# Kernel optimization log

Measured on AMD Instinct MI355X. Metric: run time of the kernel, lower is better.

Reference implementation:

```python
import jax, jax.numpy as jnp
import numpy as np

N = 50000      # nodes
E = 1600000    # edges (avg degree 32)
D = 128        # in_features
H = 2          # heads
C = 64         # out channels per head (hidden_dims[i])
HC = H * C     # concat dim per layer


def _gtc_layer(x, src, dst, Wq, bq, Wk, bk, Wv, bv, Ws, bs, gamma, beta):
    """PyG TransformerConv (concat heads, root skip) + LayerNorm."""
    n = x.shape[0]
    q = (x @ Wq + bq).reshape(n, H, C)   # [N,H,C]
    k = (x @ Wk + bk).reshape(n, H, C)
    v = (x @ Wv + bv).reshape(n, H, C)
    # per-edge attention logits: query at target, key at source
    alpha = (q[dst] * k[src]).sum(-1) * (1.0 / np.sqrt(C))  # [E,H]
    # segment softmax over incoming edges of each target node
    amax = jax.ops.segment_max(alpha, dst, num_segments=n)   # [N,H]
    ex = jnp.exp(alpha - amax[dst])                          # [E,H]
    denom = jax.ops.segment_sum(ex, dst, num_segments=n)     # [N,H]
    w = ex / denom[dst]                                      # [E,H]
    # weighted scatter-sum of source values
    out = jax.ops.segment_sum(v[src] * w[:, :, None], dst, num_segments=n)
    out = out.reshape(n, HC) + (x @ Ws + bs)  # root skip (lin_skip)
    # LayerNorm (eps=1e-5)
    mu = out.mean(-1, keepdims=True)
    var = ((out - mu) ** 2).mean(-1, keepdims=True)
    return gamma * (out - mu) / jnp.sqrt(var + 1e-5) + beta


def setup_inputs() -> dict:
    key = jax.random.key(0)
    ks = jax.random.split(key, 24)
    x = jax.random.normal(ks[0], (N, D), dtype=jnp.float32)
    edge_index = jax.random.randint(ks[1], (2, E), 0, N, dtype=jnp.int32)
    inp = {"x": x, "edge_index": edge_index}
    dims = [(D, HC), (HC, HC)]  # layer0: 128->128, layer1: 128->128
    ki = 2
    for li, (din, dout) in enumerate(dims):
        s = 1.0 / np.sqrt(din)
        for nm in ("Wq", "Wk", "Wv", "Ws"):
            inp[f"{nm}{li}"] = jax.random.uniform(ks[ki], (din, dout), jnp.float32, -s, s); ki += 1
        for nm in ("bq", "bk", "bv", "bs"):
            inp[f"{nm}{li}"] = jax.random.uniform(ks[ki], (dout,), jnp.float32, -s, s); ki += 1
        inp[f"g{li}"] = jnp.ones((dout,), jnp.float32)
        inp[f"be{li}"] = jnp.zeros((dout,), jnp.float32)
    return inp


def reference(x, edge_index,
              Wq0, Wk0, Wv0, Ws0, bq0, bk0, bv0, bs0, g0, be0,
              Wq1, Wk1, Wv1, Ws1, bq1, bk1, bv1, bs1, g1, be1):
    src, dst = edge_index[0], edge_index[1]
    h = _gtc_layer(x, src, dst, Wq0, bq0, Wk0, bk0, Wv0, bv0, Ws0, bs0, g0, be0)
    h = _gtc_layer(h, src, dst, Wq1, bq1, Wk1, bk1, Wv1, bv1, Ws1, bs1, g1, be1)
    return h
```

## Files before the change

### kernel.cpp

```cpp
#include <hip/hip_runtime.h>
#include <math.h>

#define NN 50000
#define NE 1600000
#define NBIN 391
#define BINCAP 4608
#define EPB 8192

typedef __attribute__((ext_vector_type(8))) short bf16x8;
typedef __attribute__((ext_vector_type(4))) float f32x4;
typedef __attribute__((ext_vector_type(2))) float f32x2;

__device__ __forceinline__ ushort f2bf(float f) {
  union { float f; unsigned u; } a; a.f = f;
  return (ushort)((a.u + 0x7fffu + ((a.u >> 16) & 1u)) >> 16);
}
__device__ __forceinline__ f32x2 unp2(unsigned u) {
  f32x2 r;
  r.x = __uint_as_float(u << 16);
  r.y = __uint_as_float(u & 0xffff0000u);
  return r;
}

__global__ __launch_bounds__(256) void prep_weights(
    const float* __restrict__ Wq0, const float* __restrict__ Wk0,
    const float* __restrict__ Wv0, const float* __restrict__ Ws0,
    const float* __restrict__ bq0, const float* __restrict__ bk0,
    const float* __restrict__ bv0, const float* __restrict__ bs0,
    const float* __restrict__ Wq1, const float* __restrict__ Wk1,
    const float* __restrict__ Wv1, const float* __restrict__ Ws1,
    const float* __restrict__ bq1, const float* __restrict__ bk1,
    const float* __restrict__ bv1, const float* __restrict__ bs1,
    ushort* __restrict__ Wt0, ushort* __restrict__ Wt1,
    float* __restrict__ bias0, float* __restrict__ bias1)
{
  int idx = blockIdx.x * 256 + threadIdx.x;
  if (idx >= 2 * 512 * 128) return;
  const int layer = idx >> 16;
  const int li = idx & 0xFFFF;
  const int n = li >> 7, k = li & 127, g = n >> 7, nl = n & 127;
  const float* W;
  if (layer == 0) W = g == 0 ? Wq0 : g == 1 ? Wk0 : g == 2 ? Wv0 : Ws0;
  else            W = g == 0 ? Wq1 : g == 1 ? Wk1 : g == 2 ? Wv1 : Ws1;
  (layer == 0 ? Wt0 : Wt1)[li] = f2bf(W[k * 128 + nl]);
  if (li < 512) {
    const int gb = li >> 7, nb = li & 127;
    const float* B;
    if (layer == 0) B = gb == 0 ? bq0 : gb == 1 ? bk0 : gb == 2 ? bv0 : bs0;
    else            B = gb == 0 ? bq1 : gb == 1 ? bk1 : gb == 2 ? bv1 : bs1;
    (layer == 0 ? bias0 : bias1)[li] = B[nb];
  }
}

template <int AF32>
__global__ __launch_bounds__(512) void gemm_v2(
    const void* __restrict__ Av, const ushort* __restrict__ Wt,
    const float* __restrict__ bias,
    ushort* __restrict__ q_bf, ushort* __restrict__ s_bf,
    unsigned char* __restrict__ kv8, int M)
{
  __shared__ char As[128 * 256];
  const int t = threadIdx.x;
  const int m0 = blockIdx.x * 128;

  #pragma unroll
  for (int it = 0; it < 4; ++it) {
    const int L = it * 4096 + t * 8;
    const int row = L >> 7, col = L & 127;
    const int grow = m0 + row;
    uint4 pk = make_uint4(0, 0, 0, 0);
    if (grow < M) {
      if (AF32) {
        const float* ap = (const float*)Av + (size_t)grow * 128 + col;
        const float4 a = *(const float4*)ap;
        const float4 b = *(const float4*)(ap + 4);
        pk.x = (unsigned)f2bf(a.x) | ((unsigned)f2bf(a.y) << 16);
        pk.y = (unsigned)f2bf(a.z) | ((unsigned)f2bf(a.w) << 16);
        pk.z = (unsigned)f2bf(b.x) | ((unsigned)f2bf(b.y) << 16);
        pk.w = (unsigned)f2bf(b.z) | ((unsigned)f2bf(b.w) << 16);
      } else {
        pk = *(const uint4*)((const ushort*)Av + (size_t)grow * 128 + col);
      }
    }
    const int byte = (row * 256 + col * 2) ^ ((row & 7) << 4);
    *(uint4*)(As + byte) = pk;
  }
  __syncthreads();

  const int w = t >> 6, l = t & 63, lr = l & 15, lk = l >> 4;
  const int nb = w * 64;
  const int g = w >> 1;

  bf16x8 bfr[4][4];
  #pragma unroll
  for (int ni = 0; ni < 4; ++ni)
    #pragma unroll
    for (int kk = 0; kk < 4; ++kk)
      bfr[ni][kk] = *(const bf16x8*)(Wt + (size_t)(nb + ni * 16 + lr) * 128 + kk * 32 + lk * 8);
  float4 b4[4];
  #pragma unroll
  for (int ni = 0; ni < 4; ++ni)
    b4[ni] = *(const float4*)(bias + nb + ni * 16 + lk * 4);

  #pragma unroll
  for (int mi = 0; mi < 8; ++mi) {
    const int r = mi * 16 + lr;
    bf16x8 af[4];
    #pragma unroll
    for (int kk = 0; kk < 4; ++kk) {
      const int byte = (r * 256 + (kk * 32 + lk * 8) * 2) ^ ((r & 7) << 4);
      af[kk] = *(const bf16x8*)(As + byte);
    }
    f32x4 acc[4];
    #pragma unroll
    for (int ni = 0; ni < 4; ++ni) acc[ni] = (f32x4){0.f, 0.f, 0.f, 0.f};
    #pragma unroll
    for (int kk = 0; kk < 4; ++kk)
      #pragma unroll
      for (int ni = 0; ni < 4; ++ni)
        acc[ni] = __builtin_amdgcn_mfma_f32_16x16x32_bf16(bfr[ni][kk], af[kk], acc[ni], 0, 0, 0);

    const int row = m0 + mi * 16 + lr;
    if (row < M) {
      #pragma unroll
      for (int ni = 0; ni < 4; ++ni) {
        const float v0 = acc[ni][0] + b4[ni].x;
        const float v1 = acc[ni][1] + b4[ni].y;
        const float v2 = acc[ni][2] + b4[ni].z;
        const float v3 = acc[ni][3] + b4[ni].w;
        const int c = (nb & 127) + ni * 16 + lk * 4;
        if (g == 0 || g == 3) {
          ushort4 o4;
          o4.x = f2bf(v0); o4.y = f2bf(v1); o4.z = f2bf(v2); o4.w = f2bf(v3);
          ushort* dstp = (g == 0) ? q_bf : s_bf;
          *(ushort4*)(dstp + (size_t)row * 128 + c) = o4;
        } else {
          unsigned u = __builtin_amdgcn_cvt_pk_fp8_f32(v0, v1, 0, false);
          u = __builtin_amdgcn_cvt_pk_fp8_f32(v2, v3, u, true);
          *(unsigned*)(kv8 + (size_t)row * 256 + (g == 2 ? 128 : 0) + c) = u;
        }
      }
    }
  }
}

__global__ __launch_bounds__(256) void bin_scatter(
    const int* __restrict__ src, const int* __restrict__ dst,
    int* __restrict__ binCnt, unsigned* __restrict__ binbuf, int E)
{
  __shared__ int hist[NBIN];
  __shared__ int base[NBIN];
  const int t = threadIdx.x;
  const int e0 = blockIdx.x * EPB;
  const int e1 = min(e0 + EPB, E);
  for (int i = t; i < NBIN; i += 256) hist[i] = 0;
  __syncthreads();
  for (int e = e0 + t; e < e1; e += 256) atomicAdd(&hist[dst[e] >> 7], 1);
  __syncthreads();
  for (int i = t; i < NBIN; i += 256) {
    const int c = hist[i];
    base[i] = (c > 0) ? atomicAdd(&binCnt[i], c) : 0;
    hist[i] = 0;
  }
  __syncthreads();
  for (int e = e0 + t; e < e1; e += 256) {
    const int d = dst[e], b = d >> 7;
    const int p = base[b] + atomicAdd(&hist[b], 1);
    if (p < BINCAP)
      binbuf[(size_t)b * BINCAP + p] = (unsigned)src[e] | ((unsigned)(d & 127) << 16);
  }
}

__global__ __launch_bounds__(256) void bin_fill(
    const unsigned* __restrict__ binbuf, const int* __restrict__ binCnt,
    int* __restrict__ row_start, int* __restrict__ colv)
{
  __shared__ int hist[128], scanb[128], cur[128];
  __shared__ int wred[4];
  const int b = blockIdx.x, t = threadIdx.x;
  int part = 0;
  for (int i = t; i < b; i += 256) part += min(binCnt[i], BINCAP);
  #pragma unroll
  for (int o = 32; o; o >>= 1) part += __shfl_xor(part, o, 64);
  if ((t & 63) == 0) wred[t >> 6] = part;
  const int n = min(binCnt[b], BINCAP);
  const unsigned* __restrict__ buf = binbuf + (size_t)b * BINCAP;
  if (t < 128) hist[t] = 0;
  __syncthreads();
  const int binBase = wred[0] + wred[1] + wred[2] + wred[3];
  if (b == NBIN - 1 && t == 0) row_start[NN] = binBase + n;
  for (int i = t; i < n; i += 256) atomicAdd(&hist[(buf[i] >> 16) & 127], 1);
  __syncthreads();
  if (t < 128) scanb[t] = hist[t];
  __syncthreads();
  for (int off = 1; off < 128; off <<= 1) {
    int a = (t >= off && t < 128) ? scanb[t - off] : 0;
    __syncthreads();
    if (t < 128) scanb[t] += a;
    __syncthreads();
  }
  if (t < 128) {
    const int node = b * 128 + t;
    const int base = binBase + scanb[t] - hist[t];
    if (node < NN) row_start[node] = base;
    cur[t] = base;
  }
  __syncthreads();
  for (int i = t; i < n; i += 256) {
    const unsigned v = buf[i];
    const int pos = atomicAdd(&cur[(v >> 16) & 127], 1);
    colv[pos] = (int)(v & 0xFFFFu);
  }
}

template <int WRITE_BF16>
__global__ __launch_bounds__(256) void edge_attn(
    const ushort* __restrict__ q_bf, const ushort* __restrict__ s_bf,
    const unsigned char* __restrict__ kv8,
    const int* __restrict__ row_start, const int* __restrict__ colv,
    const float* __restrict__ gamma, const float* __restrict__ beta,
    float* __restrict__ out_f, ushort* __restrict__ out_bf)
{
  const int wave = threadIdx.x >> 6, lane = threadIdx.x & 63;
  const int e8 = lane >> 3, l8 = lane & 7;
  const int n = blockIdx.x * 4 + wave;
  if (n >= NN) return;
  const int beg = row_start[n];
  const int deg = row_start[n + 1] - beg;

  int sn_own = 0;
  const bool small = (deg <= 64);
  if (small && deg > 0) sn_own = colv[beg + min(lane, deg - 1)];

  f32x2 qv[8];
  {
    const uint4 qa = *(const uint4*)(q_bf + (size_t)n * 128 + l8 * 16);
    const uint4 qb = *(const uint4*)(q_bf + (size_t)n * 128 + l8 * 16 + 8);
    qv[0] = unp2(qa.x); qv[1] = unp2(qa.y); qv[2] = unp2(qa.z); qv[3] = unp2(qa.w);
    qv[4] = unp2(qb.x); qv[5] = unp2(qb.y); qv[6] = unp2(qb.z); qv[7] = unp2(qb.w);
  }

  f32x2 acc2[8];
  #pragma unroll
  for (int j = 0; j < 8; ++j) acc2[j] = (f32x2){0.f, 0.f};
  float den = 0.f;

  #pragma unroll 4
  for (int base = 0; base < deg; base += 8) {
    const int i = base + e8;
    const int ii = min(i, deg - 1);
    const int sn = small ? __shfl(sn_own, ii, 64) : colv[beg + ii];
    const unsigned char* kvp = kv8 + (size_t)sn * 256 + l8 * 16;
    const uint4 kw = *(const uint4*)kvp;
    const uint4 vw = *(const uint4*)(kvp + 128);
    f32x2 p2 = __builtin_amdgcn_cvt_pk_f32_fp8((int)kw.x, false) * qv[0];
    p2 += __builtin_amdgcn_cvt_pk_f32_fp8((int)kw.x, true)  * qv[1];
    p2 += __builtin_amdgcn_cvt_pk_f32_fp8((int)kw.y, false) * qv[2];
    p2 += __builtin_amdgcn_cvt_pk_f32_fp8((int)kw.y, true)  * qv[3];
    p2 += __builtin_amdgcn_cvt_pk_f32_fp8((int)kw.z, false) * qv[4];
    p2 += __builtin_amdgcn_cvt_pk_f32_fp8((int)kw.z, true)  * qv[5];
    p2 += __builtin_amdgcn_cvt_pk_f32_fp8((int)kw.w, false) * qv[6];
    p2 += __builtin_amdgcn_cvt_pk_f32_fp8((int)kw.w, true)  * qv[7];
    float p = p2.x + p2.y;
    p += __shfl_xor(p, 1, 64);
    p += __shfl_xor(p, 2, 64);
    const float e = (i < deg) ? __expf(p * 0.125f) : 0.f;
    den += e;
    const f32x2 e2 = (f32x2){e, e};
    acc2[0] += __builtin_amdgcn_cvt_pk_f32_fp8((int)vw.x, false) * e2;
    acc2[1] += __builtin_amdgcn_cvt_pk_f32_fp8((int)vw.x, true)  * e2;
    acc2[2] += __builtin_amdgcn_cvt_pk_f32_fp8((int)vw.y, false) * e2;
    acc2[3] += __builtin_amdgcn_cvt_pk_f32_fp8((int)vw.y, true)  * e2;
    acc2[4] += __builtin_amdgcn_cvt_pk_f32_fp8((int)vw.z, false) * e2;
    acc2[5] += __builtin_amdgcn_cvt_pk_f32_fp8((int)vw.z, true)  * e2;
    acc2[6] += __builtin_amdgcn_cvt_pk_f32_fp8((int)vw.w, false) * e2;
    acc2[7] += __builtin_amdgcn_cvt_pk_f32_fp8((int)vw.w, true)  * e2;
  }

  #pragma unroll
  for (int off = 8; off <= 32; off <<= 1) {
    den += __shfl_xor(den, off, 64);
    #pragma unroll
    for (int j = 0; j < 8; ++j) {
      acc2[j].x += __shfl_xor(acc2[j].x, off, 64);
      acc2[j].y += __shfl_xor(acc2[j].y, off, 64);
    }
  }

  const float rden = (deg > 0) ? 1.f / den : 0.f;
  float o[16], s1 = 0.f, s2 = 0.f;
  {
    const uint4 ra = *(const uint4*)(s_bf + (size_t)n * 128 + l8 * 16);
    const uint4 rb = *(const uint4*)(s_bf + (size_t)n * 128 + l8 * 16 + 8);
    f32x2 sv[8];
    sv[0] = unp2(ra.x); sv[1] = unp2(ra.y); sv[2] = unp2(ra.z); sv[3] = unp2(ra.w);
    sv[4] = unp2(rb.x); sv[5] = unp2(rb.y); sv[6] = unp2(rb.z); sv[7] = unp2(rb.w);
    #pragma unroll
    for (int j = 0; j < 8; ++j) {
      const float a = acc2[j].x * rden + sv[j].x;
      const float b = acc2[j].y * rden + sv[j].y;
      o[2 * j] = a; o[2 * j + 1] = b;
      s1 += a + b; s2 += a * a + b * b;
    }
  }
  #pragma unroll
  for (int off = 1; off <= 4; off <<= 1) {
    s1 += __shfl_xor(s1, off, 64);
    s2 += __shfl_xor(s2, off, 64);
  }
  const float mean = s1 * (1.f / 128.f);
  const float var  = s2 * (1.f / 128.f) - mean * mean;
  const float rs   = rsqrtf(fmaxf(var, 0.f) + 1e-5f);
  if (e8 == 0) {
    const int cbase = l8 * 16;
    #pragma unroll
    for (int jj = 0; jj < 4; ++jj) {
      const float4 g4 = *(const float4*)(gamma + cbase + jj * 4);
      const float4 b4 = *(const float4*)(beta + cbase + jj * 4);
      const float r0 = g4.x * ((o[jj*4+0] - mean) * rs) + b4.x;
      const float r1 = g4.y * ((o[jj*4+1] - mean) * rs) + b4.y;
      const float r2 = g4.z * ((o[jj*4+2] - mean) * rs) + b4.z;
      const float r3 = g4.w * ((o[jj*4+3] - mean) * rs) + b4.w;
      if (WRITE_BF16) {
        ushort4 u4; u4.x = f2bf(r0); u4.y = f2bf(r1); u4.z = f2bf(r2); u4.w = f2bf(r3);
        *(ushort4*)(out_bf + (size_t)n * 128 + cbase + jj * 4) = u4;
      } else {
        *(float4*)(out_f + (size_t)n * 128 + cbase + jj * 4) = make_float4(r0, r1, r2, r3);
      }
    }
  }
}

extern "C" void kernel_launch(void* const* d_in, const int* in_sizes, int n_in,
                              void* d_out, int out_size, void* d_ws, size_t ws_size,
                              hipStream_t stream)
{
  const float* x  = (const float*)d_in[0];
  const int*   ei = (const int*)d_in[1];
  const float* P[20];
  for (int i = 0; i < 20; ++i) P[i] = (const float*)d_in[2 + i];

  char* w = (char*)d_ws;
  ushort* q_bf = (ushort*)w; w += (size_t)NN * 128 * 2;
  ushort* s_bf = (ushort*)w; w += (size_t)NN * 128 * 2;
  unsigned char* kv8 = (unsigned char*)w; w += (size_t)NN * 256;
  ushort* h_bf = (ushort*)w; w += (size_t)NN * 128 * 2;
  unsigned* binbuf = (unsigned*)w; w += (size_t)NBIN * BINCAP * 4;
  int* colv = (int*)w;      w += (size_t)NE * 4;
  ushort* Wt0 = (ushort*)w; w += (size_t)512 * 128 * 2;
  ushort* Wt1 = (ushort*)w; w += (size_t)512 * 128 * 2;
  float* bias0 = (float*)w; w += 512 * 4;
  float* bias1 = (float*)w; w += 512 * 4;
  int* row_start = (int*)w; w += (size_t)(NN + 1) * 4;
  int* binCnt = (int*)w;    w += (size_t)NBIN * 4;

  const int* srcv = ei;
  const int* dstv = ei + NE;

  hipMemsetAsync(binCnt, 0, (size_t)NBIN * 4, stream);
  bin_scatter<<<(NE + EPB - 1) / EPB, 256, 0, stream>>>(srcv, dstv, binCnt, binbuf, NE);
  bin_fill<<<NBIN, 256, 0, stream>>>(binbuf, binCnt, row_start, colv);

  prep_weights<<<(2 * 512 * 128 + 255) / 256, 256, 0, stream>>>(
      P[0], P[1], P[2], P[3], P[4], P[5], P[6], P[7],
      P[10], P[11], P[12], P[13], P[14], P[15], P[16], P[17],
      Wt0, Wt1, bias0, bias1);

  const int ggrid = (NN + 127) / 128;
  const int agrid = (NN + 3) / 4;

  gemm_v2<1><<<ggrid, 512, 0, stream>>>(x, Wt0, bias0, q_bf, s_bf, kv8, NN);
  edge_attn<1><<<agrid, 256, 0, stream>>>(q_bf, s_bf, kv8, row_start, colv,
                                          P[8], P[9], nullptr, h_bf);
  gemm_v2<0><<<ggrid, 512, 0, stream>>>(h_bf, Wt1, bias1, q_bf, s_bf, kv8, NN);
  edge_attn<0><<<agrid, 256, 0, stream>>>(q_bf, s_bf, kv8, row_start, colv,
                                          P[18], P[19], (float*)d_out, nullptr);
}
```

Before: 238.3 us.

## Merge independent preprocessing kernels into fat launches and process two nodes per wave

Bin scatter and weight prep are merged into one launch, and the layer-0 GEMM and CSR bin fill are merged into another, with blocks split by blockIdx so the independent work runs concurrently. This cuts launch count and lets the two stages fill each other's idle CUs. Each wave in edge attention now handles two destination nodes. The softmax scale is folded into q with log2e so exp2f replaces __expf. The fat kernels force 512-thread blocks and a 32KB LDS footprint on the fill path, which may reduce occupancy for those blocks.

```diff
diff --git a/kernel.cpp b/kernel.cpp
--- a/kernel.cpp
+++ b/kernel.cpp
@@ -6,10 +6,15 @@
 #define NBIN 391
 #define BINCAP 4608
 #define EPB 8192
+#define SCAT_B ((NE + EPB - 1) / EPB)
+#define PREP_B (2 * 512 * 128 / 512)
+#define GEMM_B ((NN + 127) / 128)
 
 typedef __attribute__((ext_vector_type(8))) short bf16x8;
 typedef __attribute__((ext_vector_type(4))) float f32x4;
 typedef __attribute__((ext_vector_type(2))) float f32x2;
+
+struct WPtrs { const float* p[16]; };
 
 __device__ __forceinline__ ushort f2bf(float f) {
   union { float f; unsigned u; } a; a.f = f;
@@ -22,46 +27,15 @@
   return r;
 }
 
-__global__ __launch_bounds__(256) void prep_weights(
-    const float* __restrict__ Wq0, const float* __restrict__ Wk0,
-    const float* __restrict__ Wv0, const float* __restrict__ Ws0,
-    const float* __restrict__ bq0, const float* __restrict__ bk0,
-    const float* __restrict__ bv0, const float* __restrict__ bs0,
-    const float* __restrict__ Wq1, const float* __restrict__ Wk1,
-    const float* __restrict__ Wv1, const float* __restrict__ Ws1,
-    const float* __restrict__ bq1, const float* __restrict__ bk1,
-    const float* __restrict__ bv1, const float* __restrict__ bs1,
-    ushort* __restrict__ Wt0, ushort* __restrict__ Wt1,
-    float* __restrict__ bias0, float* __restrict__ bias1)
-{
-  int idx = blockIdx.x * 256 + threadIdx.x;
-  if (idx >= 2 * 512 * 128) return;
-  const int layer = idx >> 16;
-  const int li = idx & 0xFFFF;
-  const int n = li >> 7, k = li & 127, g = n >> 7, nl = n & 127;
-  const float* W;
-  if (layer == 0) W = g == 0 ? Wq0 : g == 1 ? Wk0 : g == 2 ? Wv0 : Ws0;
-  else            W = g == 0 ? Wq1 : g == 1 ? Wk1 : g == 2 ? Wv1 : Ws1;
-  (layer == 0 ? Wt0 : Wt1)[li] = f2bf(W[k * 128 + nl]);
-  if (li < 512) {
-    const int gb = li >> 7, nb = li & 127;
-    const float* B;
-    if (layer == 0) B = gb == 0 ? bq0 : gb == 1 ? bk0 : gb == 2 ? bv0 : bs0;
-    else            B = gb == 0 ? bq1 : gb == 1 ? bk1 : gb == 2 ? bv1 : bs1;
-    (layer == 0 ? bias0 : bias1)[li] = B[nb];
-  }
-}
-
 template <int AF32>
-__global__ __launch_bounds__(512) void gemm_v2(
+__device__ __forceinline__ void gemm_body(
     const void* __restrict__ Av, const ushort* __restrict__ Wt,
     const float* __restrict__ bias,
     ushort* __restrict__ q_bf, ushort* __restrict__ s_bf,
-    unsigned char* __restrict__ kv8, int M)
-{
-  __shared__ char As[128 * 256];
+    unsigned char* __restrict__ kv8, int M, char* As, int bid)
+{
   const int t = threadIdx.x;
-  const int m0 = blockIdx.x * 128;
+  const int m0 = bid * 128;
 
   #pragma unroll
   for (int it = 0; it < 4; ++it) {
@@ -144,42 +118,70 @@
   }
 }
 
-__global__ __launch_bounds__(256) void bin_scatter(
+__global__ __launch_bounds__(512) void fat_scatter_prep(
     const int* __restrict__ src, const int* __restrict__ dst,
-    int* __restrict__ binCnt, unsigned* __restrict__ binbuf, int E)
-{
-  __shared__ int hist[NBIN];
-  __shared__ int base[NBIN];
+    int* __restrict__ binCnt, unsigned* __restrict__ binbuf,
+    WPtrs wp,
+    ushort* __restrict__ Wt0, ushort* __restrict__ Wt1,
+    float* __restrict__ bias0, float* __restrict__ bias1)
+{
   const int t = threadIdx.x;
-  const int e0 = blockIdx.x * EPB;
-  const int e1 = min(e0 + EPB, E);
-  for (int i = t; i < NBIN; i += 256) hist[i] = 0;
-  __syncthreads();
-  for (int e = e0 + t; e < e1; e += 256) atomicAdd(&hist[dst[e] >> 7], 1);
-  __syncthreads();
-  for (int i = t; i < NBIN; i += 256) {
-    const int c = hist[i];
-    base[i] = (c > 0) ? atomicAdd(&binCnt[i], c) : 0;
-    hist[i] = 0;
-  }
-  __syncthreads();
-  for (int e = e0 + t; e < e1; e += 256) {
-    const int d = dst[e], b = d >> 7;
-    const int p = base[b] + atomicAdd(&hist[b], 1);
-    if (p < BINCAP)
-      binbuf[(size_t)b * BINCAP + p] = (unsigned)src[e] | ((unsigned)(d & 127) << 16);
-  }
-}
-
-__global__ __launch_bounds__(256) void bin_fill(
+  if (blockIdx.x < SCAT_B) {
+    __shared__ int hist[NBIN], base[NBIN];
+    const int e0 = blockIdx.x * EPB;
+    const int e1 = min(e0 + EPB, NE);
+    for (int i = t; i < NBIN; i += 512) hist[i] = 0;
+    __syncthreads();
+    for (int e = e0 + t; e < e1; e += 512) atomicAdd(&hist[dst[e] >> 7], 1);
+    __syncthreads();
+    for (int i = t; i < NBIN; i += 512) {
+      const int c = hist[i];
+      base[i] = (c > 0) ? atomicAdd(&binCnt[i], c) : 0;
+      hist[i] = 0;
+    }
+    __syncthreads();
+    for (int e = e0 + t; e < e1; e += 512) {
+      const int d = dst[e], b = d >> 7;
+      const int p = base[b] + atomicAdd(&hist[b], 1);
+      if (p < BINCAP)
+        binbuf[(size_t)b * BINCAP + p] = (unsigned)src[e] | ((unsigned)(d & 127) << 16);
+    }
+  } else {
+    const int idx = (blockIdx.x - SCAT_B) * 512 + t;
+    const int layer = idx >> 16;
+    const int li = idx & 0xFFFF;
+    const int n = li >> 7, k = li & 127, g = n >> 7, nl = n & 127;
+    const float* W = wp.p[layer * 8 + g];
+    (layer == 0 ? Wt0 : Wt1)[li] = f2bf(W[k * 128 + nl]);
+    if (li < 512) {
+      const int gb = li >> 7, nbv = li & 127;
+      const float* B = wp.p[layer * 8 + 4 + gb];
+      (layer == 0 ? bias0 : bias1)[li] = B[nbv];
+    }
+  }
+}
+
+__global__ __launch_bounds__(512) void fat_gemm_fill(
+    const float* __restrict__ x, const ushort* __restrict__ Wt0,
+    const float* __restrict__ bias0,
+    ushort* __restrict__ q_bf, ushort* __restrict__ s_bf,
+    unsigned char* __restrict__ kv8,
     const unsigned* __restrict__ binbuf, const int* __restrict__ binCnt,
     int* __restrict__ row_start, int* __restrict__ colv)
 {
-  __shared__ int hist[128], scanb[128], cur[128];
-  __shared__ int wred[4];
-  const int b = blockIdx.x, t = threadIdx.x;
+  __shared__ char smem[128 * 256];
+  const int t = threadIdx.x;
+  if (blockIdx.x < GEMM_B) {
+    gemm_body<1>(x, Wt0, bias0, q_bf, s_bf, kv8, NN, smem, blockIdx.x);
+    return;
+  }
+  int* hist  = (int*)smem;
+  int* scanb = hist + 128;
+  int* cur   = scanb + 128;
+  int* wred  = cur + 128;
+  const int b = blockIdx.x - GEMM_B;
   int part = 0;
-  for (int i = t; i < b; i += 256) part += min(binCnt[i], BINCAP);
+  for (int i = t; i < b; i += 512) part += min(binCnt[i], BINCAP);
   #pragma unroll
   for (int o = 32; o; o >>= 1) part += __shfl_xor(part, o, 64);
   if ((t & 63) == 0) wred[t >> 6] = part;
@@ -187,9 +189,11 @@
   const unsigned* __restrict__ buf = binbuf + (size_t)b * BINCAP;
   if (t < 128) hist[t] = 0;
   __syncthreads();
-  const int binBase = wred[0] + wred[1] + wred[2] + wred[3];
+  int binBase = 0;
+  #pragma unroll
+  for (int i = 0; i < 8; ++i) binBase += wred[i];
   if (b == NBIN - 1 && t == 0) row_start[NN] = binBase + n;
-  for (int i = t; i < n; i += 256) atomicAdd(&hist[(buf[i] >> 16) & 127], 1);
+  for (int i = t; i < n; i += 512) atomicAdd(&hist[(buf[i] >> 16) & 127], 1);
   __syncthreads();
   if (t < 128) scanb[t] = hist[t];
   __syncthreads();
@@ -206,11 +210,21 @@
     cur[t] = base;
   }
   __syncthreads();
-  for (int i = t; i < n; i += 256) {
+  for (int i = t; i < n; i += 512) {
     const unsigned v = buf[i];
     const int pos = atomicAdd(&cur[(v >> 16) & 127], 1);
     colv[pos] = (int)(v & 0xFFFFu);
   }
+}
+
+__global__ __launch_bounds__(512) void gemm_v2(
+    const ushort* __restrict__ A, const ushort* __restrict__ Wt,
+    const float* __restrict__ bias,
+    ushort* __restrict__ q_bf, ushort* __restrict__ s_bf,
+    unsigned char* __restrict__ kv8)
+{
+  __shared__ char As[128 * 256];
+  gemm_body<0>(A, Wt, bias, q_bf, s_bf, kv8, NN, As, blockIdx.x);
 }
 
 template <int WRITE_BF16>
@@ -223,109 +237,115 @@
 {
   const int wave = threadIdx.x >> 6, lane = threadIdx.x & 63;
   const int e8 = lane >> 3, l8 = lane & 7;
-  const int n = blockIdx.x * 4 + wave;
-  if (n >= NN) return;
-  const int beg = row_start[n];
-  const int deg = row_start[n + 1] - beg;
-
-  int sn_own = 0;
-  const bool small = (deg <= 64);
-  if (small && deg > 0) sn_own = colv[beg + min(lane, deg - 1)];
-
-  f32x2 qv[8];
-  {
-    const uint4 qa = *(const uint4*)(q_bf + (size_t)n * 128 + l8 * 16);
-    const uint4 qb = *(const uint4*)(q_bf + (size_t)n * 128 + l8 * 16 + 8);
-    qv[0] = unp2(qa.x); qv[1] = unp2(qa.y); qv[2] = unp2(qa.z); qv[3] = unp2(qa.w);
-    qv[4] = unp2(qb.x); qv[5] = unp2(qb.y); qv[6] = unp2(qb.z); qv[7] = unp2(qb.w);
-  }
-
-  f32x2 acc2[8];
-  #pragma unroll
-  for (int j = 0; j < 8; ++j) acc2[j] = (f32x2){0.f, 0.f};
-  float den = 0.f;
-
-  #pragma unroll 4
-  for (int base = 0; base < deg; base += 8) {
-    const int i = base + e8;
-    const int ii = min(i, deg - 1);
-    const int sn = small ? __shfl(sn_own, ii, 64) : colv[beg + ii];
-    const unsigned char* kvp = kv8 + (size_t)sn * 256 + l8 * 16;
-    const uint4 kw = *(const uint4*)kvp;
-    const uint4 vw = *(const uint4*)(kvp + 128);
-    f32x2 p2 = __builtin_amdgcn_cvt_pk_f32_fp8((int)kw.x, false) * qv[0];
-    p2 += __builtin_amdgcn_cvt_pk_f32_fp8((int)kw.x, true)  * qv[1];
-    p2 += __builtin_amdgcn_cvt_pk_f32_fp8((int)kw.y, false) * qv[2];
-    p2 += __builtin_amdgcn_cvt_pk_f32_fp8((int)kw.y, true)  * qv[3];
-    p2 += __builtin_amdgcn_cvt_pk_f32_fp8((int)kw.z, false) * qv[4];
-    p2 += __builtin_amdgcn_cvt_pk_f32_fp8((int)kw.z, true)  * qv[5];
-    p2 += __builtin_amdgcn_cvt_pk_f32_fp8((int)kw.w, false) * qv[6];
-    p2 += __builtin_amdgcn_cvt_pk_f32_fp8((int)kw.w, true)  * qv[7];
-    float p = p2.x + p2.y;
-    p += __shfl_xor(p, 1, 64);
-    p += __shfl_xor(p, 2, 64);
-    const float e = (i < deg) ? __expf(p * 0.125f) : 0.f;
-    den += e;
-    const f32x2 e2 = (f32x2){e, e};
-    acc2[0] += __builtin_amdgcn_cvt_pk_f32_fp8((int)vw.x, false) * e2;
-    acc2[1] += __builtin_amdgcn_cvt_pk_f32_fp8((int)vw.x, true)  * e2;
-    acc2[2] += __builtin_amdgcn_cvt_pk_f32_fp8((int)vw.y, false) * e2;
-    acc2[3] += __builtin_amdgcn_cvt_pk_f32_fp8((int)vw.y, true)  * e2;
-    acc2[4] += __builtin_amdgcn_cvt_pk_f32_fp8((int)vw.z, false) * e2;
-    acc2[5] += __builtin_amdgcn_cvt_pk_f32_fp8((int)vw.z, true)  * e2;
-    acc2[6] += __builtin_amdgcn_cvt_pk_f32_fp8((int)vw.w, false) * e2;
-    acc2[7] += __builtin_amdgcn_cvt_pk_f32_fp8((int)vw.w, true)  * e2;
-  }
-
-  #pragma unroll
-  for (int off = 8; off <= 32; off <<= 1) {
-    den += __shfl_xor(den, off, 64);
-    #pragma unroll
-    for (int j = 0; j < 8; ++j) {
-      acc2[j].x += __shfl_xor(acc2[j].x, off, 64);
-      acc2[j].y += __shfl_xor(acc2[j].y, off, 64);
-    }
-  }
-
-  const float rden = (deg > 0) ? 1.f / den : 0.f;
-  float o[16], s1 = 0.f, s2 = 0.f;
-  {
-    const uint4 ra = *(const uint4*)(s_bf + (size_t)n * 128 + l8 * 16);
-    const uint4 rb = *(const uint4*)(s_bf + (size_t)n * 128 + l8 * 16 + 8);
-    f32x2 sv[8];
-    sv[0] = unp2(ra.x); sv[1] = unp2(ra.y); sv[2] = unp2(ra.z); sv[3] = unp2(ra.w);
-    sv[4] = unp2(rb.x); sv[5] = unp2(rb.y); sv[6] = unp2(rb.z); sv[7] = unp2(rb.w);
-    #pragma unroll
-    for (int j = 0; j < 8; ++j) {
-      const float a = acc2[j].x * rden + sv[j].x;
-      const float b = acc2[j].y * rden + sv[j].y;
-      o[2 * j] = a; o[2 * j + 1] = b;
-      s1 += a + b; s2 += a * a + b * b;
-    }
-  }
-  #pragma unroll
-  for (int off = 1; off <= 4; off <<= 1) {
-    s1 += __shfl_xor(s1, off, 64);
-    s2 += __shfl_xor(s2, off, 64);
-  }
-  const float mean = s1 * (1.f / 128.f);
-  const float var  = s2 * (1.f / 128.f) - mean * mean;
-  const float rs   = rsqrtf(fmaxf(var, 0.f) + 1e-5f);
-  if (e8 == 0) {
-    const int cbase = l8 * 16;
-    #pragma unroll
-    for (int jj = 0; jj < 4; ++jj) {
-      const float4 g4 = *(const float4*)(gamma + cbase + jj * 4);
-      const float4 b4 = *(const float4*)(beta + cbase + jj * 4);
-      const float r0 = g4.x * ((o[jj*4+0] - mean) * rs) + b4.x;
-      const float r1 = g4.y * ((o[jj*4+1] - mean) * rs) + b4.y;
-      const float r2 = g4.z * ((o[jj*4+2] - mean) * rs) + b4.z;
-      const float r3 = g4.w * ((o[jj*4+3] - mean) * rs) + b4.w;
-      if (WRITE_BF16) {
-        ushort4 u4; u4.x = f2bf(r0); u4.y = f2bf(r1); u4.z = f2bf(r2); u4.w = f2bf(r3);
-        *(ushort4*)(out_bf + (size_t)n * 128 + cbase + jj * 4) = u4;
-      } else {
-        *(float4*)(out_f + (size_t)n * 128 + cbase + jj * 4) = make_float4(r0, r1, r2, r3);
+  const int n0 = (blockIdx.x * 4 + wave) * 2;
+  const float QSC = 0.125f * 1.44269504f;
+
+  for (int n = n0; n < n0 + 2; ++n) {
+    if (n >= NN) return;
+    const int beg = row_start[n];
+    const int deg = row_start[n + 1] - beg;
+
+    int sn_own = 0;
+    const bool small = (deg <= 64);
+    if (small && deg > 0) sn_own = colv[beg + min(lane, deg - 1)];
+
+    f32x2 qv[8];
+    {
+      const uint4 qa = *(const uint4*)(q_bf + (size_t)n * 128 + l8 * 16);
+      const uint4 qb = *(const uint4*)(q_bf + (size_t)n * 128 + l8 * 16 + 8);
+      qv[0] = unp2(qa.x); qv[1] = unp2(qa.y); qv[2] = unp2(qa.z); qv[3] = unp2(qa.w);
+      qv[4] = unp2(qb.x); qv[5] = unp2(qb.y); qv[6] = unp2(qb.z); qv[7] = unp2(qb.w);
+      #pragma unroll
+      for (int j = 0; j < 8; ++j) qv[j] *= QSC;
+    }
+
+    f32x2 acc2[8];
+    #pragma unroll
+    for (int j = 0; j < 8; ++j) acc2[j] = (f32x2){0.f, 0.f};
+    float den = 0.f;
+
+    #pragma unroll 4
+    for (int base = 0; base < deg; base += 8) {
+      const int i = base + e8;
+      const int ii = min(i, deg - 1);
+      const int sn = small ? __shfl(sn_own, ii, 64) : colv[beg + ii];
+      const unsigned char* kvp = kv8 + (size_t)sn * 256 + l8 * 16;
+      const uint4 kw = *(const uint4*)kvp;
+      const uint4 vw = *(const uint4*)(kvp + 128);
+      f32x2 p2 = __builtin_amdgcn_cvt_pk_f32_fp8((int)kw.x, false) * qv[0];
+      p2 += __builtin_amdgcn_cvt_pk_f32_fp8((int)kw.x, true)  * qv[1];
+      p2 += __builtin_amdgcn_cvt_pk_f32_fp8((int)kw.y, false) * qv[2];
+      p2 += __builtin_amdgcn_cvt_pk_f32_fp8((int)kw.y, true)  * qv[3];
+      p2 += __builtin_amdgcn_cvt_pk_f32_fp8((int)kw.z, false) * qv[4];
+      p2 += __builtin_amdgcn_cvt_pk_f32_fp8((int)kw.z, true)  * qv[5];
+      p2 += __builtin_amdgcn_cvt_pk_f32_fp8((int)kw.w, false) * qv[6];
+      p2 += __builtin_amdgcn_cvt_pk_f32_fp8((int)kw.w, true)  * qv[7];
+      float p = p2.x + p2.y;
+      p += __shfl_xor(p, 1, 64);
+      p += __shfl_xor(p, 2, 64);
+      const float e = (i < deg) ? exp2f(p) : 0.f;
+      den += e;
+      const f32x2 e2 = (f32x2){e, e};
+      acc2[0] += __builtin_amdgcn_cvt_pk_f32_fp8((int)vw.x, false) * e2;
+      acc2[1] += __builtin_amdgcn_cvt_pk_f32_fp8((int)vw.x, true)  * e2;
+      acc2[2] += __builtin_amdgcn_cvt_pk_f32_fp8((int)vw.y, false) * e2;
+      acc2[3] += __builtin_amdgcn_cvt_pk_f32_fp8((int)vw.y, true)  * e2;
+      acc2[4] += __builtin_amdgcn_cvt_pk_f32_fp8((int)vw.z, false) * e2;
+      acc2[5] += __builtin_amdgcn_cvt_pk_f32_fp8((int)vw.z, true)  * e2;
+      acc2[6] += __builtin_amdgcn_cvt_pk_f32_fp8((int)vw.w, false) * e2;
+      acc2[7] += __builtin_amdgcn_cvt_pk_f32_fp8((int)vw.w, true)  * e2;
+    }
+
+    #pragma unroll
+    for (int off = 8; off <= 32; off <<= 1) {
+      den += __shfl_xor(den, off, 64);
+      #pragma unroll
+      for (int j = 0; j < 8; ++j) {
+        acc2[j].x += __shfl_xor(acc2[j].x, off, 64);
+        acc2[j].y += __shfl_xor(acc2[j].y, off, 64);
+      }
+    }
+
+    const float rden = (deg > 0) ? 1.f / den : 0.f;
+    float o[16], s1 = 0.f, s2 = 0.f;
+    {
+      const uint4 ra = *(const uint4*)(s_bf + (size_t)n * 128 + l8 * 16);
+      const uint4 rb = *(const uint4*)(s_bf + (size_t)n * 128 + l8 * 16 + 8);
+      f32x2 sv[8];
+      sv[0] = unp2(ra.x); sv[1] = unp2(ra.y); sv[2] = unp2(ra.z); sv[3] = unp2(ra.w);
+      sv[4] = unp2(rb.x); sv[5] = unp2(rb.y); sv[6] = unp2(rb.z); sv[7] = unp2(rb.w);
+      #pragma unroll
+      for (int j = 0; j < 8; ++j) {
+        const float a = acc2[j].x * rden + sv[j].x;
+        const float b = acc2[j].y * rden + sv[j].y;
+        o[2 * j] = a; o[2 * j + 1] = b;
+        s1 += a + b; s2 += a * a + b * b;
+      }
+    }
+    #pragma unroll
+    for (int off = 1; off <= 4; off <<= 1) {
+      s1 += __shfl_xor(s1, off, 64);
+      s2 += __shfl_xor(s2, off, 64);
+    }
+    const float mean = s1 * (1.f / 128.f);
+    const float var  = s2 * (1.f / 128.f) - mean * mean;
+    const float rs   = rsqrtf(fmaxf(var, 0.f) + 1e-5f);
+    if (e8 == 0) {
+      const int cbase = l8 * 16;
+      #pragma unroll
+      for (int jj = 0; jj < 4; ++jj) {
+        const float4 g4 = *(const float4*)(gamma + cbase + jj * 4);
+        const float4 b4 = *(const float4*)(beta + cbase + jj * 4);
+        const float r0 = g4.x * ((o[jj*4+0] - mean) * rs) + b4.x;
+        const float r1 = g4.y * ((o[jj*4+1] - mean) * rs) + b4.y;
+        const float r2 = g4.z * ((o[jj*4+2] - mean) * rs) + b4.z;
+        const float r3 = g4.w * ((o[jj*4+3] - mean) * rs) + b4.w;
+        if (WRITE_BF16) {
+          ushort4 u4; u4.x = f2bf(r0); u4.y = f2bf(r1); u4.z = f2bf(r2); u4.w = f2bf(r3);
+          *(ushort4*)(out_bf + (size_t)n * 128 + cbase + jj * 4) = u4;
+        } else {
+          *(float4*)(out_f + (size_t)n * 128 + cbase + jj * 4) = make_float4(r0, r1, r2, r3);
+        }
       }
     }
   }
@@ -357,22 +377,23 @@
   const int* srcv = ei;
   const int* dstv = ei + NE;
 
+  WPtrs wp;
+  for (int i = 0; i < 8; ++i)  wp.p[i] = P[i];
+  for (int i = 0; i < 8; ++i)  wp.p[8 + i] = P[10 + i];
+
   hipMemsetAsync(binCnt, 0, (size_t)NBIN * 4, stream);
-  bin_scatter<<<(NE + EPB - 1) / EPB, 256, 0, stream>>>(srcv, dstv, binCnt, binbuf, NE);
-  bin_fill<<<NBIN, 256, 0, stream>>>(binbuf, binCnt, row_start, colv);
-
-  prep_weights<<<(2 * 512 * 128 + 255) / 256, 256, 0, stream>>>(
-      P[0], P[1], P[2], P[3], P[4], P[5], P[6], P[7],
-      P[10], P[11], P[12], P[13], P[14], P[15], P[16], P[17],
-      Wt0, Wt1, bias0, bias1);
-
-  const int ggrid = (NN + 127) / 128;
-  const int agrid = (NN + 3) / 4;
-
-  gemm_v2<1><<<ggrid, 512, 0, stream>>>(x, Wt0, bias0, q_bf, s_bf, kv8, NN);
+
+  fat_scatter_prep<<<SCAT_B + PREP_B, 512, 0, stream>>>(
+      srcv, dstv, binCnt, binbuf, wp, Wt0, Wt1, bias0, bias1);
+
+  fat_gemm_fill<<<GEMM_B + NBIN, 512, 0, stream>>>(
+      x, Wt0, bias0, q_bf, s_bf, kv8, binbuf, binCnt, row_start, colv);
+
+  const int agrid = (NN + 7) / 8;
+
   edge_attn<1><<<agrid, 256, 0, stream>>>(q_bf, s_bf, kv8, row_start, colv,
                                           P[8], P[9], nullptr, h_bf);
-  gemm_v2<0><<<ggrid, 512, 0, stream>>>(h_bf, Wt1, bias1, q_bf, s_bf, kv8, NN);
+  gemm_v2<<<GEMM_B, 512, 0, stream>>>(h_bf, Wt1, bias1, q_bf, s_bf, kv8);
   edge_attn<0><<<agrid, 256, 0, stream>>>(q_bf, s_bf, kv8, row_start, colv,
                                           P[18], P[19], (float*)d_out, nullptr);
 }
```

New measurement: 223.2 us. 1.07x faster.
